# Optimization experiments

Hardware: AMD Instinct MI355X
Metric: run time of the kernel (lower is better)

Reference implementation:

```python
import jax, jax.numpy as jnp
import numpy as np

B, L, D = 2, 2048, 2048
H, G, HS = 32, 8, 64  # n_heads, n_query_groups, head_size
NEG = -1e30


def setup_inputs() -> dict:
    key = jax.random.key(0)
    ks = jax.random.split(key, 7)
    s = 1.0 / np.sqrt(D)
    return {
        "x": jax.random.normal(ks[0], (B, L, D), jnp.float32),
        "cos": jax.random.uniform(ks[1], (L, HS), jnp.float32),
        "sin": jax.random.uniform(ks[2], (L, HS), jnp.float32),
        "Wq": jax.random.normal(ks[3], (D, D), jnp.float32) * s,
        "Wk": jax.random.normal(ks[4], (G * HS, D), jnp.float32) * s,
        "Wv": jax.random.normal(ks[5], (G * HS, D), jnp.float32) * s,
        "Wo": jax.random.normal(ks[6], (D, D), jnp.float32) * s,
    }


def _apply_rope(t, cos, sin):
    # t: (B, h, L, HS); cos/sin: (L, HS) broadcast over (B, h)
    x1, x2 = t[..., : HS // 2], t[..., HS // 2 :]
    rotated = jnp.concatenate((-x2, x1), axis=-1)
    return (t * cos + rotated * sin).astype(t.dtype)


def reference(x, cos, sin, Wq, Wk, Wv, Wo):
    # projections (torch Linear: y = x @ W.T)
    q = jnp.einsum("bld,ed->ble", x, Wq).reshape(B, L, H, HS).transpose(0, 2, 1, 3)
    k = jnp.einsum("bld,ed->ble", x, Wk).reshape(B, L, G, HS).transpose(0, 2, 1, 3)
    v = jnp.einsum("bld,ed->ble", x, Wv).reshape(B, L, G, HS).transpose(0, 2, 1, 3)
    q = _apply_rope(q, cos, sin)
    k = _apply_rope(k, cos, sin)
    # GQA expand: each group repeated H//G consecutive times (matches expand+reshape)
    k = jnp.repeat(k, H // G, axis=1)
    v = jnp.repeat(v, H // G, axis=1)
    scale = 1.0 / np.sqrt(HS)
    scores = jnp.einsum("bhqd,bhkd->bhqk", q, k) * scale
    causal = jnp.tril(jnp.ones((L, L), bool))
    scores = jnp.where(causal, scores, NEG)
    attn = jax.nn.softmax(scores, axis=-1)
    o = jnp.einsum("bhqk,bhkd->bhqd", attn, v)  # (B,H,L,HS)
    o = o.transpose(0, 2, 1, 3).reshape(B, L, D)
    return jnp.einsum("bld,ed->ble", o, Wo)
```

## Files before the change

### kernel.cpp

```cpp
#include <hip/hip_runtime.h>

typedef __bf16 bf16;
typedef __bf16 bf16x4 __attribute__((ext_vector_type(4)));
typedef __bf16 bf16x8 __attribute__((ext_vector_type(8)));
typedef float  f32x4  __attribute__((ext_vector_type(4)));
typedef float  f32x16 __attribute__((ext_vector_type(16)));

#define GLDS16(gsrc, ldst)                                                    \
  __builtin_amdgcn_global_load_lds(                                          \
      (const __attribute__((address_space(1))) void*)(gsrc),                 \
      (__attribute__((address_space(3))) void*)(ldst), 16, 0, 0)

#define MFMA16(a, b, c) __builtin_amdgcn_mfma_f32_16x16x32_bf16((a), (b), (c), 0, 0, 0)
#define MFMA32(a, b, c) __builtin_amdgcn_mfma_f32_32x32x16_bf16((a), (b), (c), 0, 0, 0)
#define PLSWAP(a, b) asm volatile("v_permlane32_swap_b32 %0, %1" : "+v"(a), "+v"(b))

__device__ inline unsigned pk2(float a, float b) {
  union { bf16 h[2]; unsigned u; } t;
  t.h[0] = (bf16)a; t.h[1] = (bf16)b;
  return t.u;
}

__global__ __launch_bounds__(256) void cvt_kernel(const float* __restrict__ in,
                                                  bf16* __restrict__ out, int n4) {
  int i = blockIdx.x * 256 + threadIdx.x;
  if (i >= n4) return;
  f32x4 f = *(const f32x4*)(in + (size_t)i * 4);
  bf16x4 b;
#pragma unroll
  for (int j = 0; j < 4; ++j) b[j] = (bf16)f[j];
  *(bf16x4*)(out + (size_t)i * 4) = b;
}

__global__ __launch_bounds__(256) void vtr_kernel(const bf16* __restrict__ v,
                                                  bf16* __restrict__ vt) {
  constexpr int L = 2048, QS = 3072;
  const int kv0 = blockIdx.x * 64;
  const int bg = blockIdx.y;
  const int tid = threadIdx.x;
  __shared__ bf16 t[64 * 64];

#pragma unroll
  for (int i = 0; i < 2; ++i) {
    int c = tid + 256 * i;
    int kv = c >> 3, e = c & 7;
    bf16x8 row = *(const bf16x8*)(v + (size_t)((bg >> 3) * L + kv0 + kv) * QS +
                                  (bg & 7) * 64 + e * 8);
#pragma unroll
    for (int j = 0; j < 8; ++j)
      t[(8 * e + j) * 64 + (kv ^ (8 * (e ^ j)))] = row[j];
  }
  __syncthreads();

  const int d = tid >> 2, c4 = tid & 3;
  bf16* orow = vt + ((size_t)bg * 64 + d) * L + kv0;
#pragma unroll
  for (int dl = 0; dl < 2; ++dl) {
    int sc = 2 * c4 + dl;
    bf16x8 ch = *(const bf16x8*)&t[d * 64 + 8 * (sc ^ (d >> 3))];
    *(bf16x8*)(orow + 8 * sc) = ch;
  }
}

template <typename OutT, bool ROPE>
__global__ __launch_bounds__(256) void gemm_bt(const bf16* __restrict__ A,
                                               const bf16* __restrict__ Bm,
                                               OutT* __restrict__ C,
                                               int M, int N, int K,
                                               const float* __restrict__ cosb,
                                               const float* __restrict__ sinb) {
  __shared__ bf16 a_lds[128 * 32];
  __shared__ bf16 b_lds[128 * 32];
  const int tid = threadIdx.x;
  const int w = tid >> 6, lane = tid & 63;
  const int lr = lane & 15, lg = lane >> 4;
  const int wr = w >> 1, wc = w & 1;
  const int m0 = blockIdx.y * 128, n0 = blockIdx.x * 128;

  f32x4 acc[4][4];
#pragma unroll
  for (int i = 0; i < 4; ++i)
#pragma unroll
    for (int j = 0; j < 4; ++j) acc[i][j] = f32x4{0.f, 0.f, 0.f, 0.f};

  for (int kt = 0; kt < K; kt += 32) {
#pragma unroll
    for (int i = 0; i < 2; ++i) {
      int c = tid + 256 * i;
      int row = c >> 2, kc = c & 3;
      GLDS16(A  + (size_t)(m0 + row) * K + kt + kc * 8, &a_lds[(w * 64 + 256 * i) * 8]);
      GLDS16(Bm + (size_t)(n0 + row) * K + kt + kc * 8, &b_lds[(w * 64 + 256 * i) * 8]);
    }
    __syncthreads();
    bf16x8 af[4], bfr[4];
#pragma unroll
    for (int t = 0; t < 4; ++t) {
      af[t]  = *(const bf16x8*)&a_lds[(wr * 64 + t * 16 + lr) * 32 + lg * 8];
      bfr[t] = *(const bf16x8*)&b_lds[(wc * 64 + t * 16 + lr) * 32 + lg * 8];
    }
#pragma unroll
    for (int mt = 0; mt < 4; ++mt)
#pragma unroll
      for (int nt = 0; nt < 4; ++nt)
        acc[mt][nt] = MFMA16(af[mt], bfr[nt], acc[mt][nt]);
    __syncthreads();
  }

  const int hb = (n0 + wc * 64) >> 6;
  const bool dorope = ROPE && (hb < 40);
  const float rsc = (ROPE && hb < 32) ? 0.18033688011112042f : 1.0f;

#pragma unroll
  for (int mt = 0; mt < 4; ++mt)
#pragma unroll
    for (int r = 0; r < 4; ++r) {
      int mm = m0 + wr * 64 + mt * 16 + 4 * lg + r;
      float ov[4];
      if (dorope) {
        int l = mm & 2047;
        const float* cp = cosb + l * 64 + lr;
        const float* sp = sinb + l * 64 + lr;
        float a0 = acc[mt][0][r], a1 = acc[mt][1][r];
        float a2 = acc[mt][2][r], a3 = acc[mt][3][r];
        ov[0] = (a0 * cp[0]  - a2 * sp[0])  * rsc;
        ov[1] = (a1 * cp[16] - a3 * sp[16]) * rsc;
        ov[2] = (a2 * cp[32] + a0 * sp[32]) * rsc;
        ov[3] = (a3 * cp[48] + a1 * sp[48]) * rsc;
      } else {
#pragma unroll
        for (int nt = 0; nt < 4; ++nt) ov[nt] = acc[mt][nt][r];
      }
#pragma unroll
      for (int nt = 0; nt < 4; ++nt) {
        int nn = n0 + wc * 64 + nt * 16 + lr;
        C[(size_t)mm * N + nn] = (OutT)ov[nt];
      }
    }
}

__global__ __launch_bounds__(256, 4) void attn_kernel(const bf16* __restrict__ q,
                                                      const bf16* __restrict__ k,
                                                      const bf16* __restrict__ vtg,
                                                      bf16* __restrict__ o) {
  constexpr int L = 2048;
  constexpr int QS = 3072;
  constexpr int OS = 2048;
  const int id = blockIdx.x;
  const int bh = id & 63;
  const int pq = (id >> 6) & 3;
  const int gq = id >> 8;
  const int u  = (int)((0x78695A4B3C2D1E0FULL >> (4 * ((pq << 2) | gq))) & 15);
  const int q0 = u * 128;
  const int b = bh >> 5, h = bh & 31, g = h >> 2;
  const int tid = threadIdx.x;
  const int w = tid >> 6, lane = tid & 63;
  const int lc = lane & 31;
  const int H  = lane >> 5;
  const int off4 = 4 * H;
  const int qw = q0 + w * 32;
  const int qg = qw + lc;

  __shared__ bf16 k_lds[2][64 * 64];
  __shared__ bf16 vt_lds[2][64 * 64];

  bf16x8 qf[4];
  {
    const bf16* qrow = q + (size_t)(b * L + qg) * QS + h * 64 + 8 * H;
#pragma unroll
    for (int s = 0; s < 4; ++s) qf[s] = *(const bf16x8*)(qrow + 16 * s);
  }

  f32x16 acc0, acc1;
#pragma unroll
  for (int r = 0; r < 16; ++r) { acc0[r] = 0.f; acc1[r] = 0.f; }
  float m_run = -1e30f, l_run = 0.f;

  const bf16* vbase = vtg + (size_t)(b * 8 + g) * 64 * L;

  auto stageK = [&](int kv0, int buf) {
#pragma unroll
    for (int i = 0; i < 2; ++i) {
      int c = tid + 256 * i;
      int kvr = c >> 3, c8 = c & 7;
      GLDS16(k + (size_t)(b * L + kv0 + kvr) * QS + g * 64 + ((c8 ^ (kvr & 7)) * 8),
             &k_lds[buf][(w * 64 + 256 * i) * 8]);
    }
  };
  auto stageV = [&](int kv0, int buf) {
#pragma unroll
    for (int i = 0; i < 2; ++i) {
      int c = tid + 256 * i;
      GLDS16(vbase + (size_t)(c >> 3) * L + kv0 + (c & 7) * 8,
             &vt_lds[buf][(w * 64 + 256 * i) * 8]);
    }
  };

  const int nt = 2 * u + 2;
  stageK(0, 0);
  stageV(0, 0);
  __syncthreads();

  for (int it = 0; it < nt; ++it) {
    const int cur = it & 1;
    const int kv0 = it * 64;
    const bool notlast = (it + 1 < nt);
    if (notlast) {
      stageK(kv0 + 64, cur ^ 1);
      stageV(kv0 + 64, cur ^ 1);
    }

    if (kv0 <= qw + 31) {
      f32x16 p0, p1;
#pragma unroll
      for (int r = 0; r < 16; ++r) { p0[r] = 0.f; p1[r] = 0.f; }
      __builtin_amdgcn_s_setprio(1);
#pragma unroll
      for (int s = 0; s < 4; ++s) {
        int ch = ((2 * s + H) ^ (lc & 7)) * 8;
        bf16x8 kf0 = *(const bf16x8*)&k_lds[cur][lc * 64 + ch];
        bf16x8 kf1 = *(const bf16x8*)&k_lds[cur][(32 + lc) * 64 + ch];
        p0 = MFMA32(kf0, qf[s], p0);
        p1 = MFMA32(kf1, qf[s], p1);
      }
      __builtin_amdgcn_s_setprio(0);

      if (kv0 + 63 > qw) {
#pragma unroll
        for (int r = 0; r < 16; ++r) {
          int kvl = kv0 + (r & 3) + 8 * (r >> 2) + off4;
          if (kvl > qg)      p0[r] = -1e30f;
          if (kvl + 32 > qg) p1[r] = -1e30f;
        }
      }

      float mt = -1e30f;
#pragma unroll
      for (int r = 0; r < 16; ++r) mt = fmaxf(mt, fmaxf(p0[r], p1[r]));
      mt = fmaxf(mt, __shfl_xor(mt, 32));
      const int defer = __all(mt <= m_run + 11.0f);
      float alpha = 1.f;
      if (!defer) {
        float mn = fmaxf(m_run, mt);
        alpha = exp2f(m_run - mn);
        m_run = mn;
      }
      float ls = 0.f;
#pragma unroll
      for (int r = 0; r < 16; ++r) {
        p0[r] = exp2f(p0[r] - m_run);
        p1[r] = exp2f(p1[r] - m_run);
        ls += p0[r] + p1[r];
      }
      ls += __shfl_xor(ls, 32);
      l_run = l_run * alpha + ls;
      if (!defer) {
#pragma unroll
        for (int r = 0; r < 16; ++r) {
          float aq = __shfl(alpha, ((r & 3) + 8 * (r >> 2)) + off4);
          acc0[r] *= aq;
          acc1[r] *= aq;
        }
      }

      unsigned A[16];
#pragma unroll
      for (int i = 0; i < 8; ++i) {
        A[i]     = pk2(p0[2 * i], p0[2 * i + 1]);
        A[8 + i] = pk2(p1[2 * i], p1[2 * i + 1]);
      }
#pragma unroll
      for (int base = 0; base < 16; base += 4) {
        PLSWAP(A[base],     A[base + 2]);
        PLSWAP(A[base + 1], A[base + 3]);
      }

      __builtin_amdgcn_s_setprio(1);
#pragma unroll
      for (int sp = 0; sp < 4; ++sp) {
        union { unsigned u[4]; bf16x8 v8; } pa;
#pragma unroll
        for (int jx = 0; jx < 4; ++jx) pa.u[jx] = A[4 * sp + jx];
        int ch = ((2 * sp + H) ^ (lc & 7)) * 8;
        bf16x8 vf0 = *(const bf16x8*)&vt_lds[cur][lc * 64 + ch];
        bf16x8 vf1 = *(const bf16x8*)&vt_lds[cur][(32 + lc) * 64 + ch];
        acc0 = MFMA32(pa.v8, vf0, acc0);
        acc1 = MFMA32(pa.v8, vf1, acc1);
      }
      __builtin_amdgcn_s_setprio(0);
    }

    __syncthreads();
  }

#pragma unroll
  for (int r = 0; r < 16; ++r) {
    int qrow = (r & 3) + 8 * (r >> 2) + off4;
    float lq = __shfl(l_run, qrow);
    float inv = 1.f / lq;
    size_t orow = (size_t)(b * L + qw + qrow) * OS + h * 64;
    o[orow + lc]      = (bf16)(acc0[r] * inv);
    o[orow + 32 + lc] = (bf16)(acc1[r] * inv);
  }
}

extern "C" void kernel_launch(void* const* d_in, const int* in_sizes, int n_in,
                              void* d_out, int out_size, void* d_ws, size_t ws_size,
                              hipStream_t stream) {
  (void)in_sizes; (void)n_in; (void)out_size; (void)ws_size;
  const float* x    = (const float*)d_in[0];
  const float* cosb = (const float*)d_in[1];
  const float* sinb = (const float*)d_in[2];
  const float* Wq   = (const float*)d_in[3];
  const float* Wk   = (const float*)d_in[4];
  const float* Wv   = (const float*)d_in[5];
  const float* Wo   = (const float*)d_in[6];

  constexpr int B = 2, L = 2048, D = 2048, H = 32, G = 8;
  constexpr int M = B * L;
  constexpr int DKV = G * 64;
  constexpr int NQKV = D + 2 * DKV;

  char* p = (char*)d_ws;
  bf16* xb   = (bf16*)p; p += (size_t)M * D * 2;
  bf16* wqkv = (bf16*)p; p += (size_t)NQKV * D * 2;
  bf16* wob  = (bf16*)p; p += (size_t)D * D * 2;
  bf16* qkv  = (bf16*)p; p += (size_t)M * NQKV * 2;
  bf16* vtg  = (bf16*)p; p += (size_t)B * G * 64 * L * 2;
  bf16* ob   = xb;

  auto cvt = [&](const float* src, bf16* dst, size_t n) {
    int n4 = (int)(n / 4);
    cvt_kernel<<<(n4 + 255) / 256, 256, 0, stream>>>(src, dst, n4);
  };
  cvt(x,  xb,                           (size_t)M * D);
  cvt(Wq, wqkv,                         (size_t)D * D);
  cvt(Wk, wqkv + (size_t)D * D,         (size_t)DKV * D);
  cvt(Wv, wqkv + (size_t)(D + DKV) * D, (size_t)DKV * D);
  cvt(Wo, wob,                          (size_t)D * D);

  gemm_bt<bf16, true><<<dim3(NQKV / 128, M / 128), 256, 0, stream>>>(
      xb, wqkv, qkv, M, NQKV, D, cosb, sinb);

  vtr_kernel<<<dim3(L / 64, B * G), 256, 0, stream>>>(qkv + D + DKV, vtg);

  attn_kernel<<<dim3(1024), 256, 0, stream>>>(qkv, qkv + D, vtg, ob);

  gemm_bt<float, false><<<dim3(D / 128, M / 128), 256, 0, stream>>>(
      ob, wob, (float*)d_out, M, D, D, nullptr, nullptr);
}
```

Before: 242.0 us.

## Split long causal attention rows across KV halves with combine kernel; fuse conversions

Query tiles u=7..15 (the ones with the longest causal KV ranges) are each split into two blocks that process half of the KV tiles. Each half writes an unnormalised partial output plus its running max and sum, and a new combine kernel merges the two halves with a log-sum-exp rescale. Short tiles still run unsplit, and the blocks are ordered longest-first to even out the per-block work on the GPU. The five fp32-to-bf16 conversion launches are also merged into one kernel. The cost is more workspace, an extra launch, and bf16 rounding of the unnormalised partial outputs.

```diff
diff --git a/kernel.cpp b/kernel.cpp
--- a/kernel.cpp
+++ b/kernel.cpp
@@ -21,15 +21,26 @@
   return t.u;
 }
 
-__global__ __launch_bounds__(256) void cvt_kernel(const float* __restrict__ in,
-                                                  bf16* __restrict__ out, int n4) {
+__global__ __launch_bounds__(256) void cvt5_kernel(const float* __restrict__ x,
+                                                   const float* __restrict__ wq,
+                                                   const float* __restrict__ wk,
+                                                   const float* __restrict__ wv,
+                                                   const float* __restrict__ wo,
+                                                   bf16* __restrict__ xb,
+                                                   bf16* __restrict__ wqkv,
+                                                   bf16* __restrict__ wob) {
   int i = blockIdx.x * 256 + threadIdx.x;
-  if (i >= n4) return;
-  f32x4 f = *(const f32x4*)(in + (size_t)i * 4);
-  bf16x4 b;
-#pragma unroll
-  for (int j = 0; j < 4; ++j) b[j] = (bf16)f[j];
-  *(bf16x4*)(out + (size_t)i * 4) = b;
+  const float* src; bf16* dst; int off;
+  if (i < 2097152)      { src = x;  dst = xb;             off = i; }
+  else if (i < 3145728) { src = wq; dst = wqkv;           off = i - 2097152; }
+  else if (i < 3407872) { src = wk; dst = wqkv + 4194304; off = i - 3145728; }
+  else if (i < 3670016) { src = wv; dst = wqkv + 5242880; off = i - 3407872; }
+  else                  { src = wo; dst = wob;            off = i - 3670016; }
+  f32x4 f = *(const f32x4*)(src + (size_t)off * 4);
+  bf16x4 o4;
+#pragma unroll
+  for (int j = 0; j < 4; ++j) o4[j] = (bf16)f[j];
+  *(bf16x4*)(dst + (size_t)off * 4) = o4;
 }
 
 __global__ __launch_bounds__(256) void vtr_kernel(const bf16* __restrict__ v,
@@ -141,15 +152,35 @@
 __global__ __launch_bounds__(256, 4) void attn_kernel(const bf16* __restrict__ q,
                                                       const bf16* __restrict__ k,
                                                       const bf16* __restrict__ vtg,
-                                                      bf16* __restrict__ o) {
+                                                      bf16* __restrict__ o,
+                                                      bf16* __restrict__ opart,
+                                                      float* __restrict__ mpart,
+                                                      float* __restrict__ lpart,
+                                                      int split_n, int umax) {
   constexpr int L = 2048;
   constexpr int QS = 3072;
   constexpr int OS = 2048;
   const int id = blockIdx.x;
-  const int bh = id & 63;
-  const int pq = (id >> 6) & 3;
-  const int gq = id >> 8;
-  const int u  = (int)((0x78695A4B3C2D1E0FULL >> (4 * ((pq << 2) | gq))) & 15);
+  int bh, u, ts, te, pidx;
+  bool split;
+  if (id < split_n) {
+    bh = id & 63;
+    int t = id >> 6;
+    u = 15 - (t >> 1);
+    int s = t & 1;
+    ts = s * (u + 1);
+    te = ts + (u + 1);
+    pidx = (bh * 9 + (u - 7)) * 2 + s;
+    split = true;
+  } else {
+    int e = id - split_n;
+    bh = e & 63;
+    u = umax - (e >> 6);
+    ts = 0;
+    te = 2 * u + 2;
+    pidx = 0;
+    split = false;
+  }
   const int q0 = u * 128;
   const int b = bh >> 5, h = bh & 31, g = h >> 2;
   const int tid = threadIdx.x;
@@ -195,15 +226,14 @@
     }
   };
 
-  const int nt = 2 * u + 2;
-  stageK(0, 0);
-  stageV(0, 0);
+  stageK(ts * 64, 0);
+  stageV(ts * 64, 0);
   __syncthreads();
 
-  for (int it = 0; it < nt; ++it) {
-    const int cur = it & 1;
+  for (int it = ts; it < te; ++it) {
+    const int cur = (it - ts) & 1;
     const int kv0 = it * 64;
-    const bool notlast = (it + 1 < nt);
+    const bool notlast = (it + 1 < te);
     if (notlast) {
       stageK(kv0 + 64, cur ^ 1);
       stageV(kv0 + 64, cur ^ 1);
@@ -292,21 +322,69 @@
     __syncthreads();
   }
 
-#pragma unroll
-  for (int r = 0; r < 16; ++r) {
-    int qrow = (r & 3) + 8 * (r >> 2) + off4;
-    float lq = __shfl(l_run, qrow);
-    float inv = 1.f / lq;
-    size_t orow = (size_t)(b * L + qw + qrow) * OS + h * 64;
-    o[orow + lc]      = (bf16)(acc0[r] * inv);
-    o[orow + 32 + lc] = (bf16)(acc1[r] * inv);
+  if (split) {
+    bf16* op = opart + (size_t)pidx * (128 * 64);
+#pragma unroll
+    for (int r = 0; r < 16; ++r) {
+      int qrow = w * 32 + (r & 3) + 8 * (r >> 2) + off4;
+      op[qrow * 64 + lc]      = (bf16)acc0[r];
+      op[qrow * 64 + 32 + lc] = (bf16)acc1[r];
+    }
+    if (H == 0) {
+      mpart[(size_t)pidx * 128 + w * 32 + lc] = m_run;
+      lpart[(size_t)pidx * 128 + w * 32 + lc] = l_run;
+    }
+  } else {
+#pragma unroll
+    for (int r = 0; r < 16; ++r) {
+      int qrow = (r & 3) + 8 * (r >> 2) + off4;
+      float lq = __shfl(l_run, qrow);
+      float inv = 1.f / lq;
+      size_t orow = (size_t)(b * L + qw + qrow) * OS + h * 64;
+      o[orow + lc]      = (bf16)(acc0[r] * inv);
+      o[orow + 32 + lc] = (bf16)(acc1[r] * inv);
+    }
+  }
+}
+
+__global__ __launch_bounds__(256) void comb_kernel(const bf16* __restrict__ opart,
+                                                   const float* __restrict__ mpart,
+                                                   const float* __restrict__ lpart,
+                                                   bf16* __restrict__ o) {
+  constexpr int L = 2048, OS = 2048;
+  const int blk = blockIdx.x;
+  const int bh = blk / 9, uu = blk % 9, u = uu + 7;
+  const int b = bh >> 5, h = bh & 31;
+  const int q0 = u * 128;
+  const int t = threadIdx.x;
+  const int row = t >> 1, dh = (t & 1) * 32;
+
+  const size_t s0 = (size_t)blk * 2, s1 = s0 + 1;
+  float m0 = mpart[s0 * 128 + row], m1 = mpart[s1 * 128 + row];
+  float l0 = lpart[s0 * 128 + row], l1 = lpart[s1 * 128 + row];
+  float m = fmaxf(m0, m1);
+  float w0 = exp2f(m0 - m), w1 = exp2f(m1 - m);
+  float inv = 1.f / (l0 * w0 + l1 * w1);
+
+  const bf16* O0 = opart + s0 * (128 * 64) + row * 64 + dh;
+  const bf16* O1 = opart + s1 * (128 * 64) + row * 64 + dh;
+  bf16* orow = o + (size_t)(b * L + q0 + row) * OS + h * 64 + dh;
+#pragma unroll
+  for (int j = 0; j < 4; ++j) {
+    bf16x8 a = *(const bf16x8*)(O0 + 8 * j);
+    bf16x8 c = *(const bf16x8*)(O1 + 8 * j);
+    bf16x8 r;
+#pragma unroll
+    for (int e = 0; e < 8; ++e)
+      r[e] = (bf16)(((float)a[e] * w0 + (float)c[e] * w1) * inv);
+    *(bf16x8*)(orow + 8 * j) = r;
   }
 }
 
 extern "C" void kernel_launch(void* const* d_in, const int* in_sizes, int n_in,
                               void* d_out, int out_size, void* d_ws, size_t ws_size,
                               hipStream_t stream) {
-  (void)in_sizes; (void)n_in; (void)out_size; (void)ws_size;
+  (void)in_sizes; (void)n_in; (void)out_size;
   const float* x    = (const float*)d_in[0];
   const float* cosb = (const float*)d_in[1];
   const float* sinb = (const float*)d_in[2];
@@ -321,29 +399,33 @@
   constexpr int NQKV = D + 2 * DKV;
 
   char* p = (char*)d_ws;
-  bf16* xb   = (bf16*)p; p += (size_t)M * D * 2;
-  bf16* wqkv = (bf16*)p; p += (size_t)NQKV * D * 2;
-  bf16* wob  = (bf16*)p; p += (size_t)D * D * 2;
-  bf16* qkv  = (bf16*)p; p += (size_t)M * NQKV * 2;
-  bf16* vtg  = (bf16*)p; p += (size_t)B * G * 64 * L * 2;
-  bf16* ob   = xb;
-
-  auto cvt = [&](const float* src, bf16* dst, size_t n) {
-    int n4 = (int)(n / 4);
-    cvt_kernel<<<(n4 + 255) / 256, 256, 0, stream>>>(src, dst, n4);
-  };
-  cvt(x,  xb,                           (size_t)M * D);
-  cvt(Wq, wqkv,                         (size_t)D * D);
-  cvt(Wk, wqkv + (size_t)D * D,         (size_t)DKV * D);
-  cvt(Wv, wqkv + (size_t)(D + DKV) * D, (size_t)DKV * D);
-  cvt(Wo, wob,                          (size_t)D * D);
+  bf16*  xb   = (bf16*)p;  p += (size_t)M * D * 2;
+  bf16*  wqkv = (bf16*)p;  p += (size_t)NQKV * D * 2;
+  bf16*  wob  = (bf16*)p;  p += (size_t)D * D * 2;
+  bf16*  qkv  = (bf16*)p;  p += (size_t)M * NQKV * 2;
+  bf16*  vtg  = (bf16*)p;  p += (size_t)B * G * 64 * L * 2;
+  bf16*  opart = (bf16*)p; p += (size_t)1152 * 128 * 64 * 2;
+  float* mpart = (float*)p; p += (size_t)1152 * 128 * 4;
+  float* lpart = (float*)p; p += (size_t)1152 * 128 * 4;
+  bf16*  ob   = xb;
+
+  const bool do_split = ws_size >= (size_t)(p - (char*)d_ws);
+
+  cvt5_kernel<<<dim3(18432), 256, 0, stream>>>(x, Wq, Wk, Wv, Wo, xb, wqkv, wob);
 
   gemm_bt<bf16, true><<<dim3(NQKV / 128, M / 128), 256, 0, stream>>>(
       xb, wqkv, qkv, M, NQKV, D, cosb, sinb);
 
   vtr_kernel<<<dim3(L / 64, B * G), 256, 0, stream>>>(qkv + D + DKV, vtg);
 
-  attn_kernel<<<dim3(1024), 256, 0, stream>>>(qkv, qkv + D, vtg, ob);
+  if (do_split) {
+    attn_kernel<<<dim3(1600), 256, 0, stream>>>(qkv, qkv + D, vtg, ob,
+                                                opart, mpart, lpart, 1152, 6);
+    comb_kernel<<<dim3(576), 256, 0, stream>>>(opart, mpart, lpart, ob);
+  } else {
+    attn_kernel<<<dim3(1024), 256, 0, stream>>>(qkv, qkv + D, vtg, ob,
+                                                opart, mpart, lpart, 0, 15);
+  }
 
   gemm_bt<float, false><<<dim3(D / 128, M / 128), 256, 0, stream>>>(
       ob, wob, (float*)d_out, M, D, D, nullptr, nullptr);
```

Measured after the change: 239.9 us. No clear change (-0.9%).
